# Kernel optimization log

Hardware: AMD Instinct MI355X
Metric: run time of the kernel (lower is better)

## Reference

```python
import jax, jax.numpy as jnp
import numpy as np

N_KEYS, PER_KEY = 8, 6
NUM_CONCEPTS = N_KEYS * PER_KEY  # 48
NUM_CLASS = 7
D_VIT, D = 768, 512
LOGIT_SCALE = 100.0


def adaptive_avg_pool_matrix(L_in: int, L_out: int) -> np.ndarray:
    """Linear operator replicating torch AdaptiveAvgPool1d: out[i] = mean(x[start_i:end_i])."""
    M = np.zeros((L_in, L_out), dtype=np.float32)
    for i in range(L_out):
        s = (i * L_in) // L_out
        e = -(((-(i + 1)) * L_in) // L_out)  # ceil((i+1)*L_in/L_out)
        M[s:e, i] = 1.0 / (e - s)
    return M


def setup_inputs() -> dict:
    key = jax.random.key(0)
    ks = jax.random.split(key, 12)
    feats = jax.random.normal(ks[0], (12, 32, 197, D_VIT), dtype=jnp.float32)
    # frozen text-side concept embeddings (CLIP text feats are ~unit norm, 512-d)
    ce = jax.random.normal(ks[1], (NUM_CONCEPTS, D), dtype=jnp.float32)
    concept_embeds = ce / jnp.linalg.norm(ce, axis=-1, keepdims=True)
    sc = 1.0 / np.sqrt(D_VIT)
    W_lin = jax.random.normal(ks[2], (D, D_VIT), dtype=jnp.float32) * sc
    b_lin = jnp.zeros((D,), dtype=jnp.float32)
    W_proj = jax.random.normal(ks[3], (D, D_VIT), dtype=jnp.float32) * sc
    scg = 1.0 / np.sqrt(3 * D)
    W_gate = jax.random.normal(ks[4], (D, 3 * D), dtype=jnp.float32) * scg
    b_gate = jnp.zeros((D,), dtype=jnp.float32)
    scu = 1.0 / np.sqrt(2 * D)
    W_upd = jax.random.normal(ks[5], (D, 2 * D), dtype=jnp.float32) * scu
    b_upd = jnp.zeros((D,), dtype=jnp.float32)
    W_cls = jax.random.normal(ks[6], (NUM_CLASS, NUM_CONCEPTS), dtype=jnp.float32) / np.sqrt(NUM_CONCEPTS)
    b_cls = jnp.zeros((NUM_CLASS,), dtype=jnp.float32)
    return {
        'feats': feats, 'concept_embeds': concept_embeds,
        'W_lin': W_lin, 'b_lin': b_lin, 'W_proj': W_proj,
        'W_gate': W_gate, 'b_gate': b_gate, 'W_upd': W_upd, 'b_upd': b_upd,
        'W_cls': W_cls, 'b_cls': b_cls,
    }


def _forward(feats, concept_embeds, W_lin, b_lin, W_proj, W_gate, b_gate, W_upd, b_upd, W_cls, b_cls):
    L, B, S, _ = feats.shape
    M = jnp.asarray(adaptive_avg_pool_matrix(S - 1, NUM_CONCEPTS))  # [196, 48]
    q0 = jnp.broadcast_to(concept_embeds[None], (B, NUM_CONCEPTS, D))

    def step(q, f):  # f: [B, 197, 768]
        cls_tok = f[:, :1, :]                                  # [B,1,768]
        pooled = jnp.einsum('bjd,ji->bid', f[:, 1:, :], M)     # [B,48,768]
        vt = jnp.concatenate([cls_tok, pooled], axis=1) @ W_lin.T + b_lin  # [B,49,512]
        attn = jax.nn.softmax(jnp.einsum('bqd,bvd->bqv', q, vt), axis=-1)
        fuse = jnp.einsum('bqv,bvd->bqd', attn, vt)            # [B,48,512]
        cls_ctx = jnp.broadcast_to(cls_tok @ W_proj.T, q.shape)
        gate = jax.nn.sigmoid(jnp.concatenate([fuse, q, cls_ctx], -1) @ W_gate.T + b_gate)
        upd = jnp.tanh(jnp.concatenate([fuse, q], -1) @ W_upd.T + b_upd)
        return gate * q + (1.0 - gate) * upd, fuse

    _, trace = jax.lax.scan(step, q0, feats)                   # trace: [12,B,48,512]

    last = trace[-1]
    vision_semantic = last / jnp.maximum(jnp.linalg.norm(last, axis=-1, keepdims=True), 1e-12)
    vs = vision_semantic.reshape(B, N_KEYS, PER_KEY, D)
    anchors = concept_embeds.reshape(N_KEYS, PER_KEY, D)
    image_logits = (LOGIT_SCALE * jnp.einsum('bkpd,kqd->bkpq', vs, anchors).mean(axis=2)).reshape(B, NUM_CONCEPTS)
    cls_logits = image_logits @ W_cls.T + b_cls
    diffs = trace[1:] - jax.lax.stop_gradient(trace[:-1])
    loss_consistency = jnp.sum(jnp.mean(diffs * diffs, axis=(1, 2, 3)))
    return cls_logits, image_logits, loss_consistency


def reference(feats, concept_embeds, W_lin, b_lin, W_proj, W_gate, b_gate, W_upd, b_upd, W_cls, b_cls):
    return _forward(feats, concept_embeds, W_lin, b_lin, W_proj, W_gate, b_gate, W_upd, b_upd, W_cls, b_cls)
```

## Files before the change

kernel.cpp:

```cpp
#include <hip/hip_runtime.h>
#include <hip/hip_bf16.h>

#define LL 12
#define BB 32
#define SS 197
#define DV 768
#define DD 512
#define CC 48
#define VV 49
#define LOSS_DEN 786432.0f

typedef unsigned short u16;
typedef unsigned int u32;
using bf16x8 = __attribute__((ext_vector_type(8))) __bf16;
using f32x4 = __attribute__((ext_vector_type(4))) float;
using u16x8 = __attribute__((ext_vector_type(8))) u16;
using u16x4 = __attribute__((ext_vector_type(4))) u16;

__device__ __forceinline__ u16 bf16h(float x) {
    u32 u = __builtin_bit_cast(u32, x);
    return (u16)((u + 0x7FFFu + ((u >> 16) & 1u)) >> 16);
}
__device__ __forceinline__ float bf2f(u16 h) {
    u32 u = ((u32)h) << 16;
    return __builtin_bit_cast(float, u);
}
__device__ __forceinline__ f32x4 mfma16(bf16x8 a, bf16x8 b, f32x4 c) {
    return __builtin_amdgcn_mfma_f32_16x16x32_bf16(a, b, c, 0, 0, 0);
}
__device__ __forceinline__ void gl_lds16(const void* g, void* s) {
    __builtin_amdgcn_global_load_lds((const __attribute__((address_space(1))) u32*)g,
                                     (__attribute__((address_space(3))) u32*)s, 16, 0, 0);
}

#define NLW (512 * 768)
#define NGW (512 * 1536)
#define NUW (512 * 1024)
#define CTX_BLKS 48
#define POOL2_BLKS (LL * BB * 2)
#define WSPLIT4_BLKS ((NLW + NGW + NUW) / 1024)
#define INITQ8_BLKS ((BB * CC * DD) / 2048)

__device__ __forceinline__ void gemm_f32_tile(const float* __restrict__ A, int lda,
                                              const float* __restrict__ W, int wstride, int K,
                                              const float* __restrict__ bias,
                                              float* __restrict__ Cout,
                                              int m0, int n0, int t, float* AsB, float* BsB) {
    float (*As)[65] = (float(*)[65])AsB;
    float (*Bs)[65] = (float(*)[65])BsB;
    int r = t >> 2;
    int kc = (t & 3) * 8;
    int tx = t & 15, ty = t >> 4;
    float acc[4][4] = {};
    for (int k0 = 0; k0 < K; k0 += 32) {
        const float4* pa = (const float4*)(A + (size_t)(m0 + r) * lda + k0 + kc);
        float4 a0 = pa[0], a1 = pa[1];
        const float4* pw = (const float4*)(W + (size_t)(n0 + r) * wstride + k0 + kc);
        float4 w0 = pw[0], w1 = pw[1];
        As[kc + 0][r] = a0.x; As[kc + 1][r] = a0.y; As[kc + 2][r] = a0.z; As[kc + 3][r] = a0.w;
        As[kc + 4][r] = a1.x; As[kc + 5][r] = a1.y; As[kc + 6][r] = a1.z; As[kc + 7][r] = a1.w;
        Bs[kc + 0][r] = w0.x; Bs[kc + 1][r] = w0.y; Bs[kc + 2][r] = w0.z; Bs[kc + 3][r] = w0.w;
        Bs[kc + 4][r] = w1.x; Bs[kc + 5][r] = w1.y; Bs[kc + 6][r] = w1.z; Bs[kc + 7][r] = w1.w;
        __syncthreads();
#pragma unroll
        for (int kk = 0; kk < 32; ++kk) {
            float a[4], b[4];
#pragma unroll
            for (int i = 0; i < 4; ++i) { a[i] = As[kk][ty * 4 + i]; b[i] = Bs[kk][tx * 4 + i]; }
#pragma unroll
            for (int i = 0; i < 4; ++i)
#pragma unroll
                for (int j = 0; j < 4; ++j) acc[i][j] += a[i] * b[j];
        }
        __syncthreads();
    }
#pragma unroll
    for (int i = 0; i < 4; ++i) {
        int m = m0 + ty * 4 + i;
#pragma unroll
        for (int j = 0; j < 4; ++j) {
            int n = n0 + tx * 4 + j;
            Cout[(size_t)m * DD + n] = acc[i][j] + (bias ? bias[n] : 0.0f);
        }
    }
}

__global__ __launch_bounds__(256) void mega_pre(const float* __restrict__ feats,
                                                const float* __restrict__ Wl,
                                                const float* __restrict__ Wg,
                                                const float* __restrict__ Wu,
                                                const float* __restrict__ Wp,
                                                const float* __restrict__ ce,
                                                u16* __restrict__ Xh, u16* __restrict__ Xl,
                                                u16* Wlh, u16* Wll, u16* Wgh, u16* Wgl,
                                                u16* Wuh, u16* Wul,
                                                u16* __restrict__ qh, u16* __restrict__ ql,
                                                float* __restrict__ loss,
                                                float* __restrict__ ctx) {
    __shared__ float smf[2 * 32 * 65];
    int bid = blockIdx.x;
    int t = threadIdx.x;
    if (bid < CTX_BLKS) {
        gemm_f32_tile(feats, SS * DV, Wp, DV, DV, nullptr, ctx,
                      (bid >> 3) * 64, (bid & 7) * 64, t, smf, smf + 32 * 65);
    } else if (bid < CTX_BLKS + POOL2_BLKS) {
        if (t >= 192) return;
        int pb = bid - CTX_BLKS;
        int lb = pb >> 1, half = pb & 1;
        const float4* fb = (const float4*)(feats + (size_t)lb * SS * DV);
        size_t xbase = (size_t)lb * VV * DV + 4 * t;
        if (half == 0) {
            float4 c = fb[t];
            float cv[4] = {c.x, c.y, c.z, c.w};
            u16x4 hh, ll2;
#pragma unroll
            for (int j = 0; j < 4; ++j) {
                u16 h = bf16h(cv[j]);
                hh[j] = h;
                ll2[j] = bf16h(cv[j] - bf2f(h));
            }
            *(u16x4*)(Xh + xbase) = hh;
            *(u16x4*)(Xl + xbase) = ll2;
        }
        int ib0 = half * 24, ib1 = ib0 + 24;
        for (int i = ib0; i < ib1; ++i) {
            int s = (i * 196) / 48;
            int e = ((i + 1) * 196 + 47) / 48;
            float4 acc = {0.f, 0.f, 0.f, 0.f};
            for (int j = s; j < e; ++j) {
                float4 v = fb[(size_t)(1 + j) * 192 + t];
                acc.x += v.x; acc.y += v.y; acc.z += v.z; acc.w += v.w;
            }
            float inv = 1.0f / (float)(e - s);
            float av[4] = {acc.x * inv, acc.y * inv, acc.z * inv, acc.w * inv};
            u16x4 hh, ll2;
#pragma unroll
            for (int j = 0; j < 4; ++j) {
                u16 h = bf16h(av[j]);
                hh[j] = h;
                ll2[j] = bf16h(av[j] - bf2f(h));
            }
            size_t o = xbase + (size_t)(1 + i) * DV;
            *(u16x4*)(Xh + o) = hh;
            *(u16x4*)(Xl + o) = ll2;
        }
    } else if (bid < CTX_BLKS + POOL2_BLKS + WSPLIT4_BLKS) {
        int i = ((bid - CTX_BLKS - POOL2_BLKS) * 256 + t) * 4;
        float4 v;
        u16 *ph, *pl;
        int j;
        if (i < NLW) { v = *(const float4*)(Wl + i); ph = Wlh; pl = Wll; j = i; }
        else if (i < NLW + NGW) { j = i - NLW; v = *(const float4*)(Wg + j); ph = Wgh; pl = Wgl; }
        else { j = i - NLW - NGW; v = *(const float4*)(Wu + j); ph = Wuh; pl = Wul; }
        float vv[4] = {v.x, v.y, v.z, v.w};
        u16x4 hh, ll2;
#pragma unroll
        for (int k = 0; k < 4; ++k) {
            u16 h = bf16h(vv[k]);
            hh[k] = h;
            ll2[k] = bf16h(vv[k] - bf2f(h));
        }
        *(u16x4*)(ph + j) = hh;
        *(u16x4*)(pl + j) = ll2;
    } else {
        int i8 = ((bid - CTX_BLKS - POOL2_BLKS - WSPLIT4_BLKS) * 256 + t) * 8;
        int src = i8 % (CC * DD);
        float4 a = *(const float4*)(ce + src);
        float4 b2 = *(const float4*)(ce + src + 4);
        float vv[8] = {a.x, a.y, a.z, a.w, b2.x, b2.y, b2.z, b2.w};
        u16x8 hh, ll2;
#pragma unroll
        for (int k = 0; k < 8; ++k) {
            u16 h = bf16h(vv[k]);
            hh[k] = h;
            ll2[k] = bf16h(vv[k] - bf2f(h));
        }
        *(u16x8*)(qh + i8) = hh;
        *(u16x8*)(ql + i8) = ll2;
        if (i8 == 0) loss[0] = 0.0f;
    }
}

__global__ __launch_bounds__(256, 2) void vt_gemm(const u16* __restrict__ Xh, const u16* __restrict__ Xl,
                                                  const u16* __restrict__ Wh, const u16* __restrict__ Wl,
                                                  const float* __restrict__ bias,
                                                  float* __restrict__ vtf,
                                                  const float* __restrict__ ctx,
                                                  const float* __restrict__ Wg,
                                                  const float* __restrict__ bg,
                                                  float* __restrict__ Cg) {
    __shared__ u16 sm[24576];
    int tid = threadIdx.x;
    if (blockIdx.x >= 1176) {
        int b2 = blockIdx.x - 1176;
        gemm_f32_tile(ctx, DD, Wg + 1024, 1536, DD, bg, Cg,
                      (b2 >> 3) * 64, (b2 & 7) * 64, tid, (float*)sm, (float*)sm + 32 * 65);
        return;
    }
    int w = tid >> 6, l = tid & 63, lr = l & 15, ls = l >> 4;
    int i = blockIdx.x, m, n;
    if (i < 1152) { int a = i >> 6, r2 = i & 63; m = 8 * a + (r2 & 7); n = r2 >> 3; }
    else { int j = i - 1152; m = 144 + (j >> 3); n = j & 7; }
    int m0 = m * 128, n0 = n * 64;
    f32x4 acc[2][4];
#pragma unroll
    for (int ii = 0; ii < 2; ++ii)
#pragma unroll
        for (int j = 0; j < 4; ++j) acc[ii][j] = f32x4{0.f, 0.f, 0.f, 0.f};

    auto stage = [&](u16* dst, int k0) {
#pragma unroll
        for (int is = 0; is < 6; ++is) {
            int q = is * 256 + tid;
            const u16* src;
            int off;
            if (is < 2)      { int qr = q;        int row = qr >> 2, sl = qr & 3; src = Xh + (size_t)(m0 + row) * DV + k0 + ((sl ^ ((row >> 1) & 3)) << 3); off = qr * 8; }
            else if (is < 4) { int qr = q - 512;  int row = qr >> 2, sl = qr & 3; src = Xl + (size_t)(m0 + row) * DV + k0 + ((sl ^ ((row >> 1) & 3)) << 3); off = 4096 + qr * 8; }
            else if (is < 5) { int qr = q - 1024; int row = qr >> 2, sl = qr & 3; src = Wh + (size_t)(n0 + row) * DV + k0 + ((sl ^ ((row >> 1) & 3)) << 3); off = 8192 + qr * 8; }
            else             { int qr = q - 1280; int row = qr >> 2, sl = qr & 3; src = Wl + (size_t)(n0 + row) * DV + k0 + ((sl ^ ((row >> 1) & 3)) << 3); off = 10240 + qr * 8; }
            gl_lds16(src, dst + off);
        }
    };

    stage(sm, 0);
    __syncthreads();
    for (int t = 0; t < 24; ++t) {
        u16* cur = sm + ((t & 1) ? 12288 : 0);
        u16* nxt = sm + ((t & 1) ? 0 : 12288);
        if (t + 1 < 24) stage(nxt, (t + 1) * 32);
        bf16x8 ah[2], al2[2], bh[4], bl2[4];
#pragma unroll
        for (int rf = 0; rf < 2; ++rf) {
            int row = 32 * w + 16 * rf + lr;
            int ro = row * 32 + ((ls ^ ((row >> 1) & 3)) << 3);
            ah[rf] = *(const bf16x8*)(cur + ro);
            al2[rf] = *(const bf16x8*)(cur + 4096 + ro);
        }
#pragma unroll
        for (int cf = 0; cf < 4; ++cf) {
            int nn = 16 * cf + lr;
            int no = nn * 32 + ((ls ^ ((nn >> 1) & 3)) << 3);
            bh[cf] = *(const bf16x8*)(cur + 8192 + no);
            bl2[cf] = *(const bf16x8*)(cur + 10240 + no);
        }
#pragma unroll
        for (int rf = 0; rf < 2; ++rf)
#pragma unroll
            for (int cf = 0; cf < 4; ++cf) {
                acc[rf][cf] = mfma16(ah[rf], bh[cf], acc[rf][cf]);
                acc[rf][cf] = mfma16(ah[rf], bl2[cf], acc[rf][cf]);
                acc[rf][cf] = mfma16(al2[rf], bh[cf], acc[rf][cf]);
            }
        __syncthreads();
    }
#pragma unroll
    for (int rf = 0; rf < 2; ++rf)
#pragma unroll
        for (int cf = 0; cf < 4; ++cf)
#pragma unroll
            for (int r = 0; r < 4; ++r) {
                int row = m0 + 32 * w + 16 * rf + 4 * ls + r;
                int col = n0 + 16 * cf + lr;
                vtf[(size_t)row * DD + col] = acc[rf][cf][r] + bias[col];
            }
}

__device__ __forceinline__ void gemm32x64(u16* sm, const u16* Ah,
                                          const u16* Wgh, const u16* Wuh,
                                          int m0, int n0, int tid,
                                          f32x4 accg[2], f32x4 accu[2]) {
    int w = tid >> 6, lane = tid & 63, lr = lane & 15, ls = lane >> 4;
    auto stage = [&](u16* buf, int k0) {
        {
            int j = tid, row = j >> 3, sl = j & 7;
            int ko = k0 + ((sl ^ (row & 7)) << 3);
            gl_lds16(Ah + (size_t)(m0 + row) * DD + ko, buf + j * 8);
        }
#pragma unroll
        for (int i2 = 0; i2 < 4; ++i2) {
            int aidx = tid + 256 * i2;
            int arr = aidx >> 9, j = aidx & 511;
            int row = j >> 3, sl = j & 7;
            int ko = k0 + ((sl ^ (row & 7)) << 3);
            const u16* src = arr ? (Wuh + (size_t)(n0 + row) * 1024 + ko)
                                 : (Wgh + (size_t)(n0 + row) * 1536 + ko);
            gl_lds16(src, buf + 2048 + arr * 4096 + j * 8);
        }
    };
    stage(sm, 0);
    __syncthreads();
    for (int t = 0; t < 8; ++t) {
        u16* cur = sm + (t & 1) * 10240;
        if (t + 1 < 8) stage(sm + ((t + 1) & 1) * 10240, (t + 1) * 64);
#pragma unroll
        for (int ks = 0; ks < 2; ++ks) {
            int slot = ks * 4 + ls;
            int n = 16 * w + lr;
            int bo = n * 64 + ((slot ^ (n & 7)) << 3);
            bf16x8 gh8 = *(const bf16x8*)(cur + 2048 + bo);
            bf16x8 uh8 = *(const bf16x8*)(cur + 6144 + bo);
#pragma unroll
            for (int rf = 0; rf < 2; ++rf) {
                int r = 16 * rf + lr;
                int ao = r * 64 + ((slot ^ (r & 7)) << 3);
                bf16x8 ah8 = *(const bf16x8*)(cur + ao);
                accg[rf] = mfma16(ah8, gh8, accg[rf]);
                accu[rf] = mfma16(ah8, uh8, accu[rf]);
            }
        }
        __syncthreads();
    }
}

__global__ __launch_bounds__(256, 3) void attn_qpart(
    const u16* __restrict__ qh, const u16* __restrict__ ql,
    const float* __restrict__ vtL,
    float* __restrict__ fcur, const float* __restrict__ fprev,
    u16* __restrict__ fh, u16* __restrict__ fl,
    float* __restrict__ loss, int do_loss,
    const u16* __restrict__ Wgh, const u16* __restrict__ Wuh,
    float* __restrict__ qg, float* __restrict__ qu) {
    __shared__ u16 sm[20480];
    int tid = threadIdx.x;
    if (blockIdx.x < 192) {
        int wgid = blockIdx.x * 4 + (tid >> 6);
        int lane = tid & 63;
        int b = wgid / 24;
        int r0 = b * CC + (wgid % 24) * 2;
        size_t o0 = (size_t)r0 * DD + lane * 8;
        u16x8 h0 = *(const u16x8*)(qh + o0), g0 = *(const u16x8*)(ql + o0);
        u16x8 h1 = *(const u16x8*)(qh + o0 + DD), g1 = *(const u16x8*)(ql + o0 + DD);
        float q0v[8], q1v[8];
#pragma unroll
        for (int j = 0; j < 8; ++j) {
            q0v[j] = bf2f(h0[j]) + bf2f(g0[j]);
            q1v[j] = bf2f(h1[j]) + bf2f(g1[j]);
        }
        const float* vf = vtL + (size_t)b * VV * DD + lane * 8;
        float m0 = -3e38f, m1 = -3e38f, s0 = 0.f, s1 = 0.f;
        float a0[8] = {}, a1[8] = {};
        for (int v = 0; v < VV; ++v) {
            float4 r0v = *(const float4*)(vf + (size_t)v * DD);
            float4 r1v = *(const float4*)(vf + (size_t)v * DD + 4);
            float rv[8] = {r0v.x, r0v.y, r0v.z, r0v.w, r1v.x, r1v.y, r1v.z, r1v.w};
            float p0 = 0.f, p1 = 0.f;
#pragma unroll
            for (int j = 0; j < 8; ++j) { p0 += q0v[j] * rv[j]; p1 += q1v[j] * rv[j]; }
#pragma unroll
            for (int off = 32; off > 0; off >>= 1) { p0 += __shfl_xor(p0, off); p1 += __shfl_xor(p1, off); }
            float nm0 = fmaxf(m0, p0);
            float sc0 = __expf(m0 - nm0), w0 = __expf(p0 - nm0);
            s0 = s0 * sc0 + w0;
            float nm1 = fmaxf(m1, p1);
            float sc1 = __expf(m1 - nm1), w1 = __expf(p1 - nm1);
            s1 = s1 * sc1 + w1;
#pragma unroll
            for (int j = 0; j < 8; ++j) {
                a0[j] = a0[j] * sc0 + w0 * rv[j];
                a1[j] = a1[j] * sc1 + w1 * rv[j];
            }
            m0 = nm0;
            m1 = nm1;
        }
        float inv0 = 1.0f / s0, inv1 = 1.0f / s1;
        float d2 = 0.f;
        float f0v[8], f1v[8];
        u16x8 oh0, ol0, oh1, ol1;
#pragma unroll
        for (int j = 0; j < 8; ++j) {
            float f = a0[j] * inv0;
            f0v[j] = f;
            u16 hh = bf16h(f);
            oh0[j] = hh;
            ol0[j] = bf16h(f - bf2f(hh));
            float f2 = a1[j] * inv1;
            f1v[j] = f2;
            u16 h2 = bf16h(f2);
            oh1[j] = h2;
            ol1[j] = bf16h(f2 - bf2f(h2));
        }
        *(float4*)(fcur + o0) = float4{f0v[0], f0v[1], f0v[2], f0v[3]};
        *(float4*)(fcur + o0 + 4) = float4{f0v[4], f0v[5], f0v[6], f0v[7]};
        *(float4*)(fcur + o0 + DD) = float4{f1v[0], f1v[1], f1v[2], f1v[3]};
        *(float4*)(fcur + o0 + DD + 4) = float4{f1v[4], f1v[5], f1v[6], f1v[7]};
        *(u16x8*)(fh + o0) = oh0;
        *(u16x8*)(fl + o0) = ol0;
        *(u16x8*)(fh + o0 + DD) = oh1;
        *(u16x8*)(fl + o0 + DD) = ol1;
        if (do_loss) {
#pragma unroll
            for (int j = 0; j < 8; ++j) {
                float d = f0v[j] - fprev[o0 + j];
                d2 += d * d;
                float e = f1v[j] - fprev[o0 + DD + j];
                d2 += e * e;
            }
#pragma unroll
            for (int off = 32; off > 0; off >>= 1) d2 += __shfl_xor(d2, off);
            if (lane == 0) atomicAdd(loss, d2);
        }
    } else {
        int tb = blockIdx.x - 192;
        int m0 = (tb >> 3) * 32, n0 = (tb & 7) * 64;
        f32x4 accg[2], accu[2];
#pragma unroll
        for (int i = 0; i < 2; ++i) { accg[i] = f32x4{0.f, 0.f, 0.f, 0.f}; accu[i] = f32x4{0.f, 0.f, 0.f, 0.f}; }
        gemm32x64(sm, qh, Wgh + 512, Wuh + 512, m0, n0, tid, accg, accu);
        int w = tid >> 6, lane = tid & 63, lr = lane & 15, ls = lane >> 4;
#pragma unroll
        for (int rf = 0; rf < 2; ++rf)
#pragma unroll
            for (int r = 0; r < 4; ++r) {
                int row = m0 + 16 * rf + 4 * ls + r;
                int col = n0 + 16 * w + lr;
                size_t o = (size_t)row * DD + col;
                qg[o] = accg[rf][r];
                qu[o] = accu[rf][r];
            }
    }
}

__global__ __launch_bounds__(256, 3) void fusepart(
    const u16* __restrict__ fhp,
    const u16* __restrict__ qhp, const u16* __restrict__ qlp,
    const u16* __restrict__ Wgh, const u16* __restrict__ Wuh,
    const float* __restrict__ qg, const float* __restrict__ qu,
    const float* __restrict__ CgL, const float* __restrict__ bu,
    u16* __restrict__ qoh, u16* __restrict__ qol) {
    __shared__ u16 sm[20480];
    int tid = threadIdx.x;
    int m0 = (blockIdx.x >> 3) * 32, n0 = (blockIdx.x & 7) * 64;
    f32x4 accg[2], accu[2];
#pragma unroll
    for (int i = 0; i < 2; ++i) { accg[i] = f32x4{0.f, 0.f, 0.f, 0.f}; accu[i] = f32x4{0.f, 0.f, 0.f, 0.f}; }
    gemm32x64(sm, fhp, Wgh, Wuh, m0, n0, tid, accg, accu);
    int w = tid >> 6, lane = tid & 63, lr = lane & 15, ls = lane >> 4;
#pragma unroll
    for (int rf = 0; rf < 2; ++rf)
#pragma unroll
        for (int r = 0; r < 4; ++r) {
            int row = m0 + 16 * rf + 4 * ls + r;
            int col = n0 + 16 * w + lr;
            int b = row / CC;
            size_t o = (size_t)row * DD + col;
            float gpre = accg[rf][r] + qg[o] + CgL[(size_t)b * DD + col];
            float upre = accu[rf][r] + qu[o] + bu[col];
            float g = 1.0f / (1.0f + __expf(-gpre));
            float u = tanhf(upre);
            float qv = bf2f(qhp[o]) + bf2f(qlp[o]);
            float qo = g * qv + (1.0f - g) * u;
            u16 hh = bf16h(qo);
            qoh[o] = hh;
            qol[o] = bf16h(qo - bf2f(hh));
        }
}

__global__ __launch_bounds__(256) void final_kernel(const float* __restrict__ fuse_last,
                                                    const float* __restrict__ ce,
                                                    const float* __restrict__ W_cls,
                                                    const float* __restrict__ b_cls,
                                                    const float* __restrict__ loss_acc,
                                                    float* __restrict__ out) {
    int b = blockIdx.x;
    int t = threadIdx.x;
    int w = t >> 6, lane = t & 63;
    __shared__ float invn[CC];
    __shared__ float img[CC];
    const float* fb = fuse_last + (size_t)b * CC * DD;
    for (int c = w; c < CC; c += 4) {
        const float* fr = fb + (size_t)c * DD + lane * 8;
        float4 a0 = *(const float4*)fr;
        float4 a1 = *(const float4*)(fr + 4);
        float ss = a0.x * a0.x + a0.y * a0.y + a0.z * a0.z + a0.w * a0.w +
                   a1.x * a1.x + a1.y * a1.y + a1.z * a1.z + a1.w * a1.w;
#pragma unroll
        for (int off = 32; off > 0; off >>= 1) ss += __shfl_xor(ss, off);
        if (lane == 0) invn[c] = 1.0f / fmaxf(sqrtf(ss), 1e-12f);
    }
    __syncthreads();
    for (int g = w; g < CC; g += 4) {
        int k = g / 6;
        const float* ar = ce + (size_t)g * DD + lane * 8;
        float4 c0 = *(const float4*)ar;
        float4 c1 = *(const float4*)(ar + 4);
        float av[8] = {c0.x, c0.y, c0.z, c0.w, c1.x, c1.y, c1.z, c1.w};
        float accp = 0.0f;
        for (int p = 0; p < 6; ++p) {
            int row = k * 6 + p;
            const float* fr = fb + (size_t)row * DD + lane * 8;
            float4 f0 = *(const float4*)fr;
            float4 f1 = *(const float4*)(fr + 4);
            float fv[8] = {f0.x, f0.y, f0.z, f0.w, f1.x, f1.y, f1.z, f1.w};
            float d = 0.0f;
#pragma unroll
            for (int j = 0; j < 8; ++j) d += fv[j] * av[j];
            accp += d * invn[row];
        }
#pragma unroll
        for (int off = 32; off > 0; off >>= 1) accp += __shfl_xor(accp, off);
        if (lane == 0) img[g] = accp * (100.0f / 6.0f);
    }
    __syncthreads();
    if (t < CC) out[BB * 7 + b * CC + t] = img[t];
    if (t < 7) {
        float sacc = b_cls[t];
        for (int c = 0; c < CC; ++c) sacc += img[c] * W_cls[t * CC + c];
        out[b * 7 + t] = sacc;
    }
    if (b == 0 && t == 0) out[BB * 7 + BB * CC] = loss_acc[0] * (1.0f / LOSS_DEN);
}

extern "C" void kernel_launch(void* const* d_in, const int* in_sizes, int n_in,
                              void* d_out, int out_size, void* d_ws, size_t ws_size,
                              hipStream_t stream) {
    const float* feats = (const float*)d_in[0];
    const float* ce = (const float*)d_in[1];
    const float* W_lin = (const float*)d_in[2];
    const float* b_lin = (const float*)d_in[3];
    const float* W_proj = (const float*)d_in[4];
    const float* W_gate = (const float*)d_in[5];
    const float* b_gate = (const float*)d_in[6];
    const float* W_upd = (const float*)d_in[7];
    const float* b_upd = (const float*)d_in[8];
    const float* W_cls = (const float*)d_in[9];
    const float* b_cls = (const float*)d_in[10];
    float* out = (float*)d_out;

    char* base = (char*)d_ws;
    size_t off = 0;
    auto alloc = [&](size_t bytes) -> char* {
        char* r = base + off;
        off += (bytes + 255) & ~(size_t)255;
        return r;
    };
    u16* Xh = (u16*)alloc((size_t)LL * BB * VV * DV * 2);
    u16* Xl = (u16*)alloc((size_t)LL * BB * VV * DV * 2);
    float* vtf = (float*)alloc((size_t)LL * BB * VV * DD * 4);
    float* ctx = (float*)alloc((size_t)LL * BB * DD * 4);
    float* Cg = (float*)alloc((size_t)LL * BB * DD * 4);
    float* fbuf0 = (float*)alloc((size_t)BB * CC * DD * 4);
    float* fbuf1 = (float*)alloc((size_t)BB * CC * DD * 4);
    float* qg = (float*)alloc((size_t)BB * CC * DD * 4);
    float* qu = (float*)alloc((size_t)BB * CC * DD * 4);
    float* loss = (float*)alloc(256);
    u16* Wlh = (u16*)alloc((size_t)NLW * 2);
    u16* Wll = (u16*)alloc((size_t)NLW * 2);
    u16* Wgh = (u16*)alloc((size_t)NGW * 2);
    u16* Wgl = (u16*)alloc((size_t)NGW * 2);
    u16* Wuh = (u16*)alloc((size_t)NUW * 2);
    u16* Wul = (u16*)alloc((size_t)NUW * 2);
    u16* fh = (u16*)alloc((size_t)BB * CC * DD * 2);
    u16* fl = (u16*)alloc((size_t)BB * CC * DD * 2);
    u16* qah = (u16*)alloc((size_t)BB * CC * DD * 2);
    u16* qal = (u16*)alloc((size_t)BB * CC * DD * 2);
    u16* qbh = (u16*)alloc((size_t)BB * CC * DD * 2);
    u16* qbl = (u16*)alloc((size_t)BB * CC * DD * 2);
    u16* qph[2] = {qah, qbh};
    u16* qpl[2] = {qal, qbl};

    mega_pre<<<CTX_BLKS + POOL2_BLKS + WSPLIT4_BLKS + INITQ8_BLKS, 256, 0, stream>>>(
        feats, W_lin, W_gate, W_upd, W_proj, ce, Xh, Xl, Wlh, Wll, Wgh, Wgl, Wuh, Wul,
        qah, qal, loss, ctx);
    vt_gemm<<<1176 + CTX_BLKS, 256, 0, stream>>>(Xh, Xl, Wlh, Wll, b_lin, vtf,
                                                 ctx, W_gate, b_gate, Cg);

    int qc = 0;
    for (int l = 0; l < LL; ++l) {
        float* fcur = (l & 1) ? fbuf1 : fbuf0;
        const float* fprev = (l & 1) ? fbuf0 : fbuf1;
        int grid = (l < LL - 1) ? 576 : 192;
        attn_qpart<<<grid, 256, 0, stream>>>(qph[qc], qpl[qc],
                                             vtf + (size_t)l * BB * VV * DD,
                                             fcur, fprev, fh, fl, loss, l > 0 ? 1 : 0,
                                             Wgh, Wuh, qg, qu);
        if (l < LL - 1) {
            fusepart<<<384, 256, 0, stream>>>(fh, qph[qc], qpl[qc],
                                              Wgh, Wuh, qg, qu,
                                              Cg + (size_t)l * BB * DD, b_upd,
                                              qph[qc ^ 1], qpl[qc ^ 1]);
            qc ^= 1;
        }
    }

    final_kernel<<<BB, 256, 0, stream>>>((LL - 1) & 1 ? fbuf1 : fbuf0, ce, W_cls, b_cls, loss, out);
}
```

Before: 798.4 us.

## Precompose gate/update weights with W_lin to hoist fuse projections out of recurrence

Since fuse is linear in the vision tokens, the gate and update contributions of fuse are rewritten as attention over pre-projected tokens VG/VU. These come from combined weights W_gate·W_lin and W_upd·W_lin, computed once in a larger batched GEMM. The per-layer fusepart kernel is removed, and each layer becomes a single layer_step kernel that rebuilds q from the previous step's pre-activations. This trades per-layer serial GEMMs for a bigger up-front parallel GEMM and more memory traffic, and the combined weights use single bf16 precision, which risks accuracy.

```diff
diff --git a/kernel.cpp b/kernel.cpp
--- a/kernel.cpp
+++ b/kernel.cpp
@@ -37,6 +37,8 @@
 #define NGW (512 * 1536)
 #define NUW (512 * 1024)
 #define CTX_BLKS 48
+#define WCOMB_BLKS 96
+#define BIAS_BLKS 1
 #define POOL2_BLKS (LL * BB * 2)
 #define WSPLIT4_BLKS ((NLW + NGW + NUW) / 1024)
 #define INITQ8_BLKS ((BB * CC * DD) / 2048)
@@ -85,27 +87,94 @@
     }
 }
 
+__device__ __forceinline__ void gemm_f32_nn(const float* __restrict__ A, int lda,
+                                            const float* __restrict__ B, int ldb, int K,
+                                            u16* __restrict__ Cbf, int ldc,
+                                            int m0, int n0, int t, float* AsB, float* BsB) {
+    float (*As)[65] = (float(*)[65])AsB;
+    float (*Bs)[68] = (float(*)[68])BsB;
+    int tx = t & 15, ty = t >> 4;
+    float acc[4][4] = {};
+    for (int k0 = 0; k0 < K; k0 += 32) {
+        {
+            int r = t >> 2, kc = (t & 3) * 8;
+            const float4* pa = (const float4*)(A + (size_t)(m0 + r) * lda + k0 + kc);
+            float4 a0 = pa[0], a1 = pa[1];
+            As[kc + 0][r] = a0.x; As[kc + 1][r] = a0.y; As[kc + 2][r] = a0.z; As[kc + 3][r] = a0.w;
+            As[kc + 4][r] = a1.x; As[kc + 5][r] = a1.y; As[kc + 6][r] = a1.z; As[kc + 7][r] = a1.w;
+        }
+        {
+            int kr = t >> 3, jc = (t & 7) * 8;
+            const float4* pb = (const float4*)(B + (size_t)(k0 + kr) * ldb + n0 + jc);
+            float4 b0 = pb[0], b1 = pb[1];
+            Bs[kr][jc + 0] = b0.x; Bs[kr][jc + 1] = b0.y; Bs[kr][jc + 2] = b0.z; Bs[kr][jc + 3] = b0.w;
+            Bs[kr][jc + 4] = b1.x; Bs[kr][jc + 5] = b1.y; Bs[kr][jc + 6] = b1.z; Bs[kr][jc + 7] = b1.w;
+        }
+        __syncthreads();
+#pragma unroll
+        for (int kk = 0; kk < 32; ++kk) {
+            float a[4], b[4];
+#pragma unroll
+            for (int i = 0; i < 4; ++i) { a[i] = As[kk][ty * 4 + i]; b[i] = Bs[kk][tx * 4 + i]; }
+#pragma unroll
+            for (int i = 0; i < 4; ++i)
+#pragma unroll
+                for (int j = 0; j < 4; ++j) acc[i][j] += a[i] * b[j];
+        }
+        __syncthreads();
+    }
+#pragma unroll
+    for (int i = 0; i < 4; ++i)
+#pragma unroll
+        for (int j = 0; j < 4; ++j)
+            Cbf[(size_t)(m0 + ty * 4 + i) * ldc + n0 + tx * 4 + j] = bf16h(acc[i][j]);
+}
+
 __global__ __launch_bounds__(256) void mega_pre(const float* __restrict__ feats,
                                                 const float* __restrict__ Wl,
                                                 const float* __restrict__ Wg,
                                                 const float* __restrict__ Wu,
                                                 const float* __restrict__ Wp,
+                                                const float* __restrict__ bl,
+                                                const float* __restrict__ bg,
+                                                const float* __restrict__ buv,
                                                 const float* __restrict__ ce,
                                                 u16* __restrict__ Xh, u16* __restrict__ Xl,
-                                                u16* Wlh, u16* Wll, u16* Wgh, u16* Wgl,
-                                                u16* Wuh, u16* Wul,
+                                                u16* Wlh, u16* Wll, u16* Wgh, u16* Wuh,
+                                                u16* Wcg, u16* Wcu,
+                                                float* __restrict__ bg2, float* __restrict__ bu2,
                                                 u16* __restrict__ qh, u16* __restrict__ ql,
                                                 float* __restrict__ loss,
                                                 float* __restrict__ ctx) {
-    __shared__ float smf[2 * 32 * 65];
+    __shared__ float smf[32 * 65 + 32 * 68];
     int bid = blockIdx.x;
     int t = threadIdx.x;
     if (bid < CTX_BLKS) {
         gemm_f32_tile(feats, SS * DV, Wp, DV, DV, nullptr, ctx,
                       (bid >> 3) * 64, (bid & 7) * 64, t, smf, smf + 32 * 65);
-    } else if (bid < CTX_BLKS + POOL2_BLKS) {
+    } else if (bid < CTX_BLKS + 2 * WCOMB_BLKS) {
+        int b2 = bid - CTX_BLKS;
+        int which = b2 >= WCOMB_BLKS;
+        int b3 = b2 - which * WCOMB_BLKS;
+        int m0 = (b3 / 12) * 64, n0 = (b3 % 12) * 64;
+        if (which == 0)
+            gemm_f32_nn(Wg, 1536, Wl, DV, 512, Wcg, DV, m0, n0, t, smf, smf + 32 * 65);
+        else
+            gemm_f32_nn(Wu, 1024, Wl, DV, 512, Wcu, DV, m0, n0, t, smf, smf + 32 * 65);
+    } else if (bid < CTX_BLKS + 2 * WCOMB_BLKS + BIAS_BLKS) {
+        for (int n = t; n < 512; n += 256) {
+            float sg = bg[n], su = buv[n];
+            for (int k = 0; k < 512; ++k) {
+                float blv = bl[k];
+                sg += Wg[(size_t)n * 1536 + k] * blv;
+                su += Wu[(size_t)n * 1024 + k] * blv;
+            }
+            bg2[n] = sg;
+            bu2[n] = su;
+        }
+    } else if (bid < CTX_BLKS + 2 * WCOMB_BLKS + BIAS_BLKS + POOL2_BLKS) {
         if (t >= 192) return;
-        int pb = bid - CTX_BLKS;
+        int pb = bid - CTX_BLKS - 2 * WCOMB_BLKS - BIAS_BLKS;
         int lb = pb >> 1, half = pb & 1;
         const float4* fb = (const float4*)(feats + (size_t)lb * SS * DV);
         size_t xbase = (size_t)lb * VV * DV + 4 * t;
@@ -144,14 +213,14 @@
             *(u16x4*)(Xh + o) = hh;
             *(u16x4*)(Xl + o) = ll2;
         }
-    } else if (bid < CTX_BLKS + POOL2_BLKS + WSPLIT4_BLKS) {
-        int i = ((bid - CTX_BLKS - POOL2_BLKS) * 256 + t) * 4;
+    } else if (bid < CTX_BLKS + 2 * WCOMB_BLKS + BIAS_BLKS + POOL2_BLKS + WSPLIT4_BLKS) {
+        int i = ((bid - CTX_BLKS - 2 * WCOMB_BLKS - BIAS_BLKS - POOL2_BLKS) * 256 + t) * 4;
         float4 v;
-        u16 *ph, *pl;
+        u16 *ph, *pl = nullptr;
         int j;
         if (i < NLW) { v = *(const float4*)(Wl + i); ph = Wlh; pl = Wll; j = i; }
-        else if (i < NLW + NGW) { j = i - NLW; v = *(const float4*)(Wg + j); ph = Wgh; pl = Wgl; }
-        else { j = i - NLW - NGW; v = *(const float4*)(Wu + j); ph = Wuh; pl = Wul; }
+        else if (i < NLW + NGW) { j = i - NLW; v = *(const float4*)(Wg + j); ph = Wgh; }
+        else { j = i - NLW - NGW; v = *(const float4*)(Wu + j); ph = Wuh; }
         float vv[4] = {v.x, v.y, v.z, v.w};
         u16x4 hh, ll2;
 #pragma unroll
@@ -161,9 +230,9 @@
             ll2[k] = bf16h(vv[k] - bf2f(h));
         }
         *(u16x4*)(ph + j) = hh;
-        *(u16x4*)(pl + j) = ll2;
+        if (pl) *(u16x4*)(pl + j) = ll2;
     } else {
-        int i8 = ((bid - CTX_BLKS - POOL2_BLKS - WSPLIT4_BLKS) * 256 + t) * 8;
+        int i8 = ((bid - CTX_BLKS - 2 * WCOMB_BLKS - BIAS_BLKS - POOL2_BLKS - WSPLIT4_BLKS) * 256 + t) * 8;
         int src = i8 % (CC * DD);
         float4 a = *(const float4*)(ce + src);
         float4 b2 = *(const float4*)(ce + src + 4);
@@ -181,24 +250,28 @@
     }
 }
 
-__global__ __launch_bounds__(256, 2) void vt_gemm(const u16* __restrict__ Xh, const u16* __restrict__ Xl,
-                                                  const u16* __restrict__ Wh, const u16* __restrict__ Wl,
-                                                  const float* __restrict__ bias,
-                                                  float* __restrict__ vtf,
-                                                  const float* __restrict__ ctx,
-                                                  const float* __restrict__ Wg,
-                                                  const float* __restrict__ bg,
-                                                  float* __restrict__ Cg) {
+__global__ __launch_bounds__(256, 2) void big_gemm(const u16* __restrict__ Xh, const u16* __restrict__ Xl,
+                                                   const u16* __restrict__ Wh, const u16* __restrict__ Wl,
+                                                   const float* __restrict__ bias,
+                                                   float* __restrict__ vtf,
+                                                   const u16* __restrict__ Wcg, const u16* __restrict__ Wcu,
+                                                   float* __restrict__ VG, float* __restrict__ VU,
+                                                   const float* __restrict__ ctx,
+                                                   const float* __restrict__ Wg,
+                                                   const float* __restrict__ bg2,
+                                                   float* __restrict__ Cg) {
     __shared__ u16 sm[24576];
     int tid = threadIdx.x;
-    if (blockIdx.x >= 1176) {
-        int b2 = blockIdx.x - 1176;
-        gemm_f32_tile(ctx, DD, Wg + 1024, 1536, DD, bg, Cg,
+    if (blockIdx.x >= 3528) {
+        int b2 = blockIdx.x - 3528;
+        gemm_f32_tile(ctx, DD, Wg + 1024, 1536, DD, bg2, Cg,
                       (b2 >> 3) * 64, (b2 & 7) * 64, tid, (float*)sm, (float*)sm + 32 * 65);
         return;
     }
+    int sub = blockIdx.x / 1176;
+    int i = blockIdx.x % 1176;
     int w = tid >> 6, l = tid & 63, lr = l & 15, ls = l >> 4;
-    int i = blockIdx.x, m, n;
+    int m, n;
     if (i < 1152) { int a = i >> 6, r2 = i & 63; m = 8 * a + (r2 & 7); n = r2 >> 3; }
     else { int j = i - 1152; m = 144 + (j >> 3); n = j & 7; }
     int m0 = m * 128, n0 = n * 64;
@@ -208,137 +281,181 @@
 #pragma unroll
         for (int j = 0; j < 4; ++j) acc[ii][j] = f32x4{0.f, 0.f, 0.f, 0.f};
 
-    auto stage = [&](u16* dst, int k0) {
-#pragma unroll
-        for (int is = 0; is < 6; ++is) {
-            int q = is * 256 + tid;
-            const u16* src;
-            int off;
-            if (is < 2)      { int qr = q;        int row = qr >> 2, sl = qr & 3; src = Xh + (size_t)(m0 + row) * DV + k0 + ((sl ^ ((row >> 1) & 3)) << 3); off = qr * 8; }
-            else if (is < 4) { int qr = q - 512;  int row = qr >> 2, sl = qr & 3; src = Xl + (size_t)(m0 + row) * DV + k0 + ((sl ^ ((row >> 1) & 3)) << 3); off = 4096 + qr * 8; }
-            else if (is < 5) { int qr = q - 1024; int row = qr >> 2, sl = qr & 3; src = Wh + (size_t)(n0 + row) * DV + k0 + ((sl ^ ((row >> 1) & 3)) << 3); off = 8192 + qr * 8; }
-            else             { int qr = q - 1280; int row = qr >> 2, sl = qr & 3; src = Wl + (size_t)(n0 + row) * DV + k0 + ((sl ^ ((row >> 1) & 3)) << 3); off = 10240 + qr * 8; }
-            gl_lds16(src, dst + off);
+    if (sub == 0) {
+        auto stage = [&](u16* dst, int k0) {
+#pragma unroll
+            for (int is = 0; is < 6; ++is) {
+                int q = is * 256 + tid;
+                const u16* src;
+                int off;
+                if (is < 2)      { int qr = q;        int row = qr >> 2, sl = qr & 3; src = Xh + (size_t)(m0 + row) * DV + k0 + ((sl ^ ((row >> 1) & 3)) << 3); off = qr * 8; }
+                else if (is < 4) { int qr = q - 512;  int row = qr >> 2, sl = qr & 3; src = Xl + (size_t)(m0 + row) * DV + k0 + ((sl ^ ((row >> 1) & 3)) << 3); off = 4096 + qr * 8; }
+                else if (is < 5) { int qr = q - 1024; int row = qr >> 2, sl = qr & 3; src = Wh + (size_t)(n0 + row) * DV + k0 + ((sl ^ ((row >> 1) & 3)) << 3); off = 8192 + qr * 8; }
+                else             { int qr = q - 1280; int row = qr >> 2, sl = qr & 3; src = Wl + (size_t)(n0 + row) * DV + k0 + ((sl ^ ((row >> 1) & 3)) << 3); off = 10240 + qr * 8; }
+                gl_lds16(src, dst + off);
+            }
+        };
+        stage(sm, 0);
+        __syncthreads();
+        for (int t = 0; t < 24; ++t) {
+            u16* cur = sm + ((t & 1) ? 12288 : 0);
+            if (t + 1 < 24) stage(sm + ((t & 1) ? 0 : 12288), (t + 1) * 32);
+            bf16x8 ah[2], al2[2], bh[4], bl2[4];
+#pragma unroll
+            for (int rf = 0; rf < 2; ++rf) {
+                int row = 32 * w + 16 * rf + lr;
+                int ro = row * 32 + ((ls ^ ((row >> 1) & 3)) << 3);
+                ah[rf] = *(const bf16x8*)(cur + ro);
+                al2[rf] = *(const bf16x8*)(cur + 4096 + ro);
+            }
+#pragma unroll
+            for (int cf = 0; cf < 4; ++cf) {
+                int nn = 16 * cf + lr;
+                int no = nn * 32 + ((ls ^ ((nn >> 1) & 3)) << 3);
+                bh[cf] = *(const bf16x8*)(cur + 8192 + no);
+                bl2[cf] = *(const bf16x8*)(cur + 10240 + no);
+            }
+#pragma unroll
+            for (int rf = 0; rf < 2; ++rf)
+#pragma unroll
+                for (int cf = 0; cf < 4; ++cf) {
+                    acc[rf][cf] = mfma16(ah[rf], bh[cf], acc[rf][cf]);
+                    acc[rf][cf] = mfma16(ah[rf], bl2[cf], acc[rf][cf]);
+                    acc[rf][cf] = mfma16(al2[rf], bh[cf], acc[rf][cf]);
+                }
+            __syncthreads();
+        }
+#pragma unroll
+        for (int rf = 0; rf < 2; ++rf)
+#pragma unroll
+            for (int cf = 0; cf < 4; ++cf)
+#pragma unroll
+                for (int r = 0; r < 4; ++r) {
+                    int row = m0 + 32 * w + 16 * rf + 4 * ls + r;
+                    int col = n0 + 16 * cf + lr;
+                    vtf[(size_t)row * DD + col] = acc[rf][cf][r] + bias[col];
+                }
+    } else {
+        const u16* Wc = (sub == 1) ? Wcg : Wcu;
+        float* Out = (sub == 1) ? VG : VU;
+        auto stage = [&](u16* dst, int k0) {
+#pragma unroll
+            for (int is = 0; is < 2; ++is) {
+                int q = is * 256 + tid;
+                int row = q >> 2, sl = q & 3;
+                gl_lds16(Xh + (size_t)(m0 + row) * DV + k0 + ((sl ^ ((row >> 1) & 3)) << 3), dst + q * 8);
+            }
+            {
+                int row = tid >> 2, sl = tid & 3;
+                gl_lds16(Wc + (size_t)(n0 + row) * DV + k0 + ((sl ^ ((row >> 1) & 3)) << 3), dst + 4096 + tid * 8);
+            }
+        };
+        stage(sm, 0);
+        __syncthreads();
+        for (int t = 0; t < 24; ++t) {
+            u16* cur = sm + (t & 1) * 6144;
+            if (t + 1 < 24) stage(sm + ((t + 1) & 1) * 6144, (t + 1) * 32);
+            bf16x8 ah[2], bh[4];
+#pragma unroll
+            for (int rf = 0; rf < 2; ++rf) {
+                int row = 32 * w + 16 * rf + lr;
+                ah[rf] = *(const bf16x8*)(cur + row * 32 + ((ls ^ ((row >> 1) & 3)) << 3));
+            }
+#pragma unroll
+            for (int cf = 0; cf < 4; ++cf) {
+                int nn = 16 * cf + lr;
+                bh[cf] = *(const bf16x8*)(cur + 4096 + nn * 32 + ((ls ^ ((nn >> 1) & 3)) << 3));
+            }
+#pragma unroll
+            for (int rf = 0; rf < 2; ++rf)
+#pragma unroll
+                for (int cf = 0; cf < 4; ++cf)
+                    acc[rf][cf] = mfma16(ah[rf], bh[cf], acc[rf][cf]);
+            __syncthreads();
+        }
+#pragma unroll
+        for (int rf = 0; rf < 2; ++rf)
+#pragma unroll
+            for (int cf = 0; cf < 4; ++cf)
+#pragma unroll
+                for (int r = 0; r < 4; ++r) {
+                    int row = m0 + 32 * w + 16 * rf + 4 * ls + r;
+                    int col = n0 + 16 * cf + lr;
+                    Out[(size_t)row * DD + col] = acc[rf][cf][r];
+                }
+    }
+}
+
+__global__ __launch_bounds__(256, 2) void layer_step(
+    const u16* __restrict__ qph, const u16* __restrict__ qpl,
+    const float* __restrict__ gpgP, const float* __restrict__ gpuP,
+    const float* __restrict__ qgP, const float* __restrict__ quP,
+    const float* __restrict__ vtL, const float* __restrict__ vgL, const float* __restrict__ vuL,
+    const float* __restrict__ CgL, const float* __restrict__ bu2,
+    float* __restrict__ fcur, const float* __restrict__ fprev, float* __restrict__ loss,
+    int do_loss, int first, int last,
+    u16* __restrict__ qoh, u16* __restrict__ qol,
+    float* __restrict__ gpgO, float* __restrict__ gpuO,
+    const u16* __restrict__ Wgh, const u16* __restrict__ Wuh,
+    float* __restrict__ qgO, float* __restrict__ quO) {
+    __shared__ u16 sm[32768];
+    int tid = threadIdx.x;
+
+    auto recon8 = [&](size_t o, float out[8]) {
+        u16x8 ph = *(const u16x8*)(qph + o), pl = *(const u16x8*)(qpl + o);
+        if (first) {
+#pragma unroll
+            for (int j = 0; j < 8; ++j) out[j] = bf2f(ph[j]) + bf2f(pl[j]);
+        } else {
+            float4 g0 = *(const float4*)(gpgP + o), g1 = *(const float4*)(gpgP + o + 4);
+            float4 u0 = *(const float4*)(gpuP + o), u1 = *(const float4*)(gpuP + o + 4);
+            float4 a0 = *(const float4*)(qgP + o), a1 = *(const float4*)(qgP + o + 4);
+            float4 b0 = *(const float4*)(quP + o), b1 = *(const float4*)(quP + o + 4);
+            float gg[8] = {g0.x, g0.y, g0.z, g0.w, g1.x, g1.y, g1.z, g1.w};
+            float uu[8] = {u0.x, u0.y, u0.z, u0.w, u1.x, u1.y, u1.z, u1.w};
+            float ag[8] = {a0.x, a0.y, a0.z, a0.w, a1.x, a1.y, a1.z, a1.w};
+            float bb[8] = {b0.x, b0.y, b0.z, b0.w, b1.x, b1.y, b1.z, b1.w};
+#pragma unroll
+            for (int j = 0; j < 8; ++j) {
+                float g = 1.0f / (1.0f + __expf(-(gg[j] + ag[j])));
+                float u = tanhf(uu[j] + bb[j]);
+                float qp = bf2f(ph[j]) + bf2f(pl[j]);
+                out[j] = g * qp + (1.0f - g) * u;
+            }
         }
     };
 
-    stage(sm, 0);
-    __syncthreads();
-    for (int t = 0; t < 24; ++t) {
-        u16* cur = sm + ((t & 1) ? 12288 : 0);
-        u16* nxt = sm + ((t & 1) ? 0 : 12288);
-        if (t + 1 < 24) stage(nxt, (t + 1) * 32);
-        bf16x8 ah[2], al2[2], bh[4], bl2[4];
-#pragma unroll
-        for (int rf = 0; rf < 2; ++rf) {
-            int row = 32 * w + 16 * rf + lr;
-            int ro = row * 32 + ((ls ^ ((row >> 1) & 3)) << 3);
-            ah[rf] = *(const bf16x8*)(cur + ro);
-            al2[rf] = *(const bf16x8*)(cur + 4096 + ro);
-        }
-#pragma unroll
-        for (int cf = 0; cf < 4; ++cf) {
-            int nn = 16 * cf + lr;
-            int no = nn * 32 + ((ls ^ ((nn >> 1) & 3)) << 3);
-            bh[cf] = *(const bf16x8*)(cur + 8192 + no);
-            bl2[cf] = *(const bf16x8*)(cur + 10240 + no);
-        }
-#pragma unroll
-        for (int rf = 0; rf < 2; ++rf)
-#pragma unroll
-            for (int cf = 0; cf < 4; ++cf) {
-                acc[rf][cf] = mfma16(ah[rf], bh[cf], acc[rf][cf]);
-                acc[rf][cf] = mfma16(ah[rf], bl2[cf], acc[rf][cf]);
-                acc[rf][cf] = mfma16(al2[rf], bh[cf], acc[rf][cf]);
-            }
-        __syncthreads();
-    }
-#pragma unroll
-    for (int rf = 0; rf < 2; ++rf)
-#pragma unroll
-        for (int cf = 0; cf < 4; ++cf)
-#pragma unroll
-            for (int r = 0; r < 4; ++r) {
-                int row = m0 + 32 * w + 16 * rf + 4 * ls + r;
-                int col = n0 + 16 * cf + lr;
-                vtf[(size_t)row * DD + col] = acc[rf][cf][r] + bias[col];
-            }
-}
-
-__device__ __forceinline__ void gemm32x64(u16* sm, const u16* Ah,
-                                          const u16* Wgh, const u16* Wuh,
-                                          int m0, int n0, int tid,
-                                          f32x4 accg[2], f32x4 accu[2]) {
-    int w = tid >> 6, lane = tid & 63, lr = lane & 15, ls = lane >> 4;
-    auto stage = [&](u16* buf, int k0) {
-        {
-            int j = tid, row = j >> 3, sl = j & 7;
-            int ko = k0 + ((sl ^ (row & 7)) << 3);
-            gl_lds16(Ah + (size_t)(m0 + row) * DD + ko, buf + j * 8);
-        }
-#pragma unroll
-        for (int i2 = 0; i2 < 4; ++i2) {
-            int aidx = tid + 256 * i2;
-            int arr = aidx >> 9, j = aidx & 511;
-            int row = j >> 3, sl = j & 7;
-            int ko = k0 + ((sl ^ (row & 7)) << 3);
-            const u16* src = arr ? (Wuh + (size_t)(n0 + row) * 1024 + ko)
-                                 : (Wgh + (size_t)(n0 + row) * 1536 + ko);
-            gl_lds16(src, buf + 2048 + arr * 4096 + j * 8);
-        }
-    };
-    stage(sm, 0);
-    __syncthreads();
-    for (int t = 0; t < 8; ++t) {
-        u16* cur = sm + (t & 1) * 10240;
-        if (t + 1 < 8) stage(sm + ((t + 1) & 1) * 10240, (t + 1) * 64);
-#pragma unroll
-        for (int ks = 0; ks < 2; ++ks) {
-            int slot = ks * 4 + ls;
-            int n = 16 * w + lr;
-            int bo = n * 64 + ((slot ^ (n & 7)) << 3);
-            bf16x8 gh8 = *(const bf16x8*)(cur + 2048 + bo);
-            bf16x8 uh8 = *(const bf16x8*)(cur + 6144 + bo);
-#pragma unroll
-            for (int rf = 0; rf < 2; ++rf) {
-                int r = 16 * rf + lr;
-                int ao = r * 64 + ((slot ^ (r & 7)) << 3);
-                bf16x8 ah8 = *(const bf16x8*)(cur + ao);
-                accg[rf] = mfma16(ah8, gh8, accg[rf]);
-                accu[rf] = mfma16(ah8, uh8, accu[rf]);
-            }
-        }
-        __syncthreads();
-    }
-}
-
-__global__ __launch_bounds__(256, 3) void attn_qpart(
-    const u16* __restrict__ qh, const u16* __restrict__ ql,
-    const float* __restrict__ vtL,
-    float* __restrict__ fcur, const float* __restrict__ fprev,
-    u16* __restrict__ fh, u16* __restrict__ fl,
-    float* __restrict__ loss, int do_loss,
-    const u16* __restrict__ Wgh, const u16* __restrict__ Wuh,
-    float* __restrict__ qg, float* __restrict__ qu) {
-    __shared__ u16 sm[20480];
-    int tid = threadIdx.x;
     if (blockIdx.x < 192) {
-        int wgid = blockIdx.x * 4 + (tid >> 6);
-        int lane = tid & 63;
-        int b = wgid / 24;
-        int r0 = b * CC + (wgid % 24) * 2;
+        int d = blockIdx.x;
+        int xcd = d & 7, tt = d >> 3;
+        int b = (tt / 6) * 8 + xcd, rg = tt % 6;
+        int wv = tid >> 6, lane = tid & 63;
+        int r0 = b * CC + rg * 8 + wv * 2;
         size_t o0 = (size_t)r0 * DD + lane * 8;
-        u16x8 h0 = *(const u16x8*)(qh + o0), g0 = *(const u16x8*)(ql + o0);
-        u16x8 h1 = *(const u16x8*)(qh + o0 + DD), g1 = *(const u16x8*)(ql + o0 + DD);
         float q0v[8], q1v[8];
-#pragma unroll
-        for (int j = 0; j < 8; ++j) {
-            q0v[j] = bf2f(h0[j]) + bf2f(g0[j]);
-            q1v[j] = bf2f(h1[j]) + bf2f(g1[j]);
+        recon8(o0, q0v);
+        recon8(o0 + DD, q1v);
+        if (!last) {
+            u16x8 h0, l0, h1, l1;
+#pragma unroll
+            for (int j = 0; j < 8; ++j) {
+                u16 h = bf16h(q0v[j]);
+                h0[j] = h;
+                l0[j] = bf16h(q0v[j] - bf2f(h));
+                u16 h2 = bf16h(q1v[j]);
+                h1[j] = h2;
+                l1[j] = bf16h(q1v[j] - bf2f(h2));
+            }
+            *(u16x8*)(qoh + o0) = h0;
+            *(u16x8*)(qol + o0) = l0;
+            *(u16x8*)(qoh + o0 + DD) = h1;
+            *(u16x8*)(qol + o0 + DD) = l1;
         }
         const float* vf = vtL + (size_t)b * VV * DD + lane * 8;
+        const float* gf = vgL + (size_t)b * VV * DD + lane * 8;
+        const float* uf = vuL + (size_t)b * VV * DD + lane * 8;
         float m0 = -3e38f, m1 = -3e38f, s0 = 0.f, s1 = 0.f;
-        float a0[8] = {}, a1[8] = {};
+        float af0[8] = {}, af1[8] = {}, ag0[8] = {}, ag1[8] = {}, au0[8] = {}, au1[8] = {};
         for (int v = 0; v < VV; ++v) {
             float4 r0v = *(const float4*)(vf + (size_t)v * DD);
             float4 r1v = *(const float4*)(vf + (size_t)v * DD + 4);
@@ -354,105 +471,145 @@
             float nm1 = fmaxf(m1, p1);
             float sc1 = __expf(m1 - nm1), w1 = __expf(p1 - nm1);
             s1 = s1 * sc1 + w1;
-#pragma unroll
-            for (int j = 0; j < 8; ++j) {
-                a0[j] = a0[j] * sc0 + w0 * rv[j];
-                a1[j] = a1[j] * sc1 + w1 * rv[j];
+            if (!last) {
+                float4 gv0 = *(const float4*)(gf + (size_t)v * DD);
+                float4 gv1 = *(const float4*)(gf + (size_t)v * DD + 4);
+                float4 uv0 = *(const float4*)(uf + (size_t)v * DD);
+                float4 uv1 = *(const float4*)(uf + (size_t)v * DD + 4);
+                float gv[8] = {gv0.x, gv0.y, gv0.z, gv0.w, gv1.x, gv1.y, gv1.z, gv1.w};
+                float uv[8] = {uv0.x, uv0.y, uv0.z, uv0.w, uv1.x, uv1.y, uv1.z, uv1.w};
+#pragma unroll
+                for (int j = 0; j < 8; ++j) {
+                    af0[j] = af0[j] * sc0 + w0 * rv[j];
+                    af1[j] = af1[j] * sc1 + w1 * rv[j];
+                    ag0[j] = ag0[j] * sc0 + w0 * gv[j];
+                    ag1[j] = ag1[j] * sc1 + w1 * gv[j];
+                    au0[j] = au0[j] * sc0 + w0 * uv[j];
+                    au1[j] = au1[j] * sc1 + w1 * uv[j];
+                }
+            } else {
+#pragma unroll
+                for (int j = 0; j < 8; ++j) {
+                    af0[j] = af0[j] * sc0 + w0 * rv[j];
+                    af1[j] = af1[j] * sc1 + w1 * rv[j];
+                }
             }
             m0 = nm0;
             m1 = nm1;
         }
         float inv0 = 1.0f / s0, inv1 = 1.0f / s1;
-        float d2 = 0.f;
         float f0v[8], f1v[8];
-        u16x8 oh0, ol0, oh1, ol1;
-#pragma unroll
-        for (int j = 0; j < 8; ++j) {
-            float f = a0[j] * inv0;
-            f0v[j] = f;
-            u16 hh = bf16h(f);
-            oh0[j] = hh;
-            ol0[j] = bf16h(f - bf2f(hh));
-            float f2 = a1[j] * inv1;
-            f1v[j] = f2;
-            u16 h2 = bf16h(f2);
-            oh1[j] = h2;
-            ol1[j] = bf16h(f2 - bf2f(h2));
-        }
+#pragma unroll
+        for (int j = 0; j < 8; ++j) { f0v[j] = af0[j] * inv0; f1v[j] = af1[j] * inv1; }
         *(float4*)(fcur + o0) = float4{f0v[0], f0v[1], f0v[2], f0v[3]};
         *(float4*)(fcur + o0 + 4) = float4{f0v[4], f0v[5], f0v[6], f0v[7]};
         *(float4*)(fcur + o0 + DD) = float4{f1v[0], f1v[1], f1v[2], f1v[3]};
         *(float4*)(fcur + o0 + DD + 4) = float4{f1v[4], f1v[5], f1v[6], f1v[7]};
-        *(u16x8*)(fh + o0) = oh0;
-        *(u16x8*)(fl + o0) = ol0;
-        *(u16x8*)(fh + o0 + DD) = oh1;
-        *(u16x8*)(fl + o0 + DD) = ol1;
         if (do_loss) {
+            float d2 = 0.f;
 #pragma unroll
             for (int j = 0; j < 8; ++j) {
-                float d = f0v[j] - fprev[o0 + j];
-                d2 += d * d;
-                float e = f1v[j] - fprev[o0 + DD + j];
-                d2 += e * e;
+                float dd = f0v[j] - fprev[o0 + j];
+                d2 += dd * dd;
+                float ee = f1v[j] - fprev[o0 + DD + j];
+                d2 += ee * ee;
             }
 #pragma unroll
             for (int off = 32; off > 0; off >>= 1) d2 += __shfl_xor(d2, off);
             if (lane == 0) atomicAdd(loss, d2);
+        }
+        if (!last) {
+            float4 c0 = *(const float4*)(CgL + (size_t)b * DD + lane * 8);
+            float4 c1 = *(const float4*)(CgL + (size_t)b * DD + lane * 8 + 4);
+            float cg[8] = {c0.x, c0.y, c0.z, c0.w, c1.x, c1.y, c1.z, c1.w};
+            float4 e0 = *(const float4*)(bu2 + lane * 8);
+            float4 e1 = *(const float4*)(bu2 + lane * 8 + 4);
+            float bv[8] = {e0.x, e0.y, e0.z, e0.w, e1.x, e1.y, e1.z, e1.w};
+            float og0[8], og1[8], ou0[8], ou1[8];
+#pragma unroll
+            for (int j = 0; j < 8; ++j) {
+                og0[j] = ag0[j] * inv0 + cg[j];
+                og1[j] = ag1[j] * inv1 + cg[j];
+                ou0[j] = au0[j] * inv0 + bv[j];
+                ou1[j] = au1[j] * inv1 + bv[j];
+            }
+            *(float4*)(gpgO + o0) = float4{og0[0], og0[1], og0[2], og0[3]};
+            *(float4*)(gpgO + o0 + 4) = float4{og0[4], og0[5], og0[6], og0[7]};
+            *(float4*)(gpgO + o0 + DD) = float4{og1[0], og1[1], og1[2], og1[3]};
+            *(float4*)(gpgO + o0 + DD + 4) = float4{og1[4], og1[5], og1[6], og1[7]};
+            *(float4*)(gpuO + o0) = float4{ou0[0], ou0[1], ou0[2], ou0[3]};
+            *(float4*)(gpuO + o0 + 4) = float4{ou0[4], ou0[5], ou0[6], ou0[7]};
+            *(float4*)(gpuO + o0 + DD) = float4{ou1[0], ou1[1], ou1[2], ou1[3]};
+            *(float4*)(gpuO + o0 + DD + 4) = float4{ou1[4], ou1[5], ou1[6], ou1[7]};
         }
     } else {
         int tb = blockIdx.x - 192;
         int m0 = (tb >> 3) * 32, n0 = (tb & 7) * 64;
+        for (int j = 0; j < 8; ++j) {
+            int e = j * 2048 + tid * 8;
+            int row = e >> 9, col = e & 511;
+            size_t o = (size_t)(m0 + row) * DD + col;
+            float qv[8];
+            recon8(o, qv);
+            u16x8 hv;
+#pragma unroll
+            for (int jj = 0; jj < 8; ++jj) hv[jj] = bf16h(qv[jj]);
+            int cslot = (col >> 3) & 7;
+            int addr = row * 512 + (col & ~63) + ((cslot ^ (row & 7)) << 3);
+            *(u16x8*)(sm + addr) = hv;
+        }
+        __syncthreads();
         f32x4 accg[2], accu[2];
 #pragma unroll
         for (int i = 0; i < 2; ++i) { accg[i] = f32x4{0.f, 0.f, 0.f, 0.f}; accu[i] = f32x4{0.f, 0.f, 0.f, 0.f}; }
-        gemm32x64(sm, qh, Wgh + 512, Wuh + 512, m0, n0, tid, accg, accu);
-        int w = tid >> 6, lane = tid & 63, lr = lane & 15, ls = lane >> 4;
+        int wv = tid >> 6, lane = tid & 63, lr = lane & 15, ls = lane >> 4;
+        u16* wbuf = sm + 16384;
+        auto stageW = [&](u16* buf, int k0) {
+#pragma unroll
+            for (int i2 = 0; i2 < 4; ++i2) {
+                int aidx = tid + 256 * i2;
+                int arr = aidx >> 9, jx = aidx & 511;
+                int row = jx >> 3, sl = jx & 7;
+                int ko = k0 + ((sl ^ (row & 7)) << 3);
+                const u16* src = arr ? (Wuh + (size_t)(n0 + row) * 1024 + 512 + ko)
+                                     : (Wgh + (size_t)(n0 + row) * 1536 + 512 + ko);
+                gl_lds16(src, buf + arr * 4096 + jx * 8);
+            }
+        };
+        stageW(wbuf, 0);
+        __syncthreads();
+        for (int t2 = 0; t2 < 8; ++t2) {
+            u16* cur = wbuf + (t2 & 1) * 8192;
+            if (t2 + 1 < 8) stageW(wbuf + ((t2 + 1) & 1) * 8192, (t2 + 1) * 64);
+#pragma unroll
+            for (int ks = 0; ks < 2; ++ks) {
+                int slot = ks * 4 + ls;
+                int n = 16 * wv + lr;
+                int bo = n * 64 + ((slot ^ (n & 7)) << 3);
+                bf16x8 gh8 = *(const bf16x8*)(cur + bo);
+                bf16x8 uh8 = *(const bf16x8*)(cur + 4096 + bo);
+#pragma unroll
+                for (int rf = 0; rf < 2; ++rf) {
+                    int r = 16 * rf + lr;
+                    int ao = r * 512 + t2 * 64 + ((slot ^ (r & 7)) << 3);
+                    bf16x8 ah8 = *(const bf16x8*)(sm + ao);
+                    accg[rf] = mfma16(ah8, gh8, accg[rf]);
+                    accu[rf] = mfma16(ah8, uh8, accu[rf]);
+                }
+            }
+            __syncthreads();
+        }
 #pragma unroll
         for (int rf = 0; rf < 2; ++rf)
 #pragma unroll
             for (int r = 0; r < 4; ++r) {
                 int row = m0 + 16 * rf + 4 * ls + r;
-                int col = n0 + 16 * w + lr;
+                int col = n0 + 16 * wv + lr;
                 size_t o = (size_t)row * DD + col;
-                qg[o] = accg[rf][r];
-                qu[o] = accu[rf][r];
-            }
-    }
-}
-
-__global__ __launch_bounds__(256, 3) void fusepart(
-    const u16* __restrict__ fhp,
-    const u16* __restrict__ qhp, const u16* __restrict__ qlp,
-    const u16* __restrict__ Wgh, const u16* __restrict__ Wuh,
-    const float* __restrict__ qg, const float* __restrict__ qu,
-    const float* __restrict__ CgL, const float* __restrict__ bu,
-    u16* __restrict__ qoh, u16* __restrict__ qol) {
-    __shared__ u16 sm[20480];
-    int tid = threadIdx.x;
-    int m0 = (blockIdx.x >> 3) * 32, n0 = (blockIdx.x & 7) * 64;
-    f32x4 accg[2], accu[2];
-#pragma unroll
-    for (int i = 0; i < 2; ++i) { accg[i] = f32x4{0.f, 0.f, 0.f, 0.f}; accu[i] = f32x4{0.f, 0.f, 0.f, 0.f}; }
-    gemm32x64(sm, fhp, Wgh, Wuh, m0, n0, tid, accg, accu);
-    int w = tid >> 6, lane = tid & 63, lr = lane & 15, ls = lane >> 4;
-#pragma unroll
-    for (int rf = 0; rf < 2; ++rf)
-#pragma unroll
-        for (int r = 0; r < 4; ++r) {
-            int row = m0 + 16 * rf + 4 * ls + r;
-            int col = n0 + 16 * w + lr;
-            int b = row / CC;
-            size_t o = (size_t)row * DD + col;
-            float gpre = accg[rf][r] + qg[o] + CgL[(size_t)b * DD + col];
-            float upre = accu[rf][r] + qu[o] + bu[col];
-            float g = 1.0f / (1.0f + __expf(-gpre));
-            float u = tanhf(upre);
-            float qv = bf2f(qhp[o]) + bf2f(qlp[o]);
-            float qo = g * qv + (1.0f - g) * u;
-            u16 hh = bf16h(qo);
-            qoh[o] = hh;
-            qol[o] = bf16h(qo - bf2f(hh));
-        }
+                qgO[o] = accg[rf][r];
+                quO[o] = accu[rf][r];
+            }
+    }
 }
 
 __global__ __launch_bounds__(256) void final_kernel(const float* __restrict__ fuse_last,
@@ -536,50 +693,56 @@
     u16* Xh = (u16*)alloc((size_t)LL * BB * VV * DV * 2);
     u16* Xl = (u16*)alloc((size_t)LL * BB * VV * DV * 2);
     float* vtf = (float*)alloc((size_t)LL * BB * VV * DD * 4);
+    float* VG = (float*)alloc((size_t)LL * BB * VV * DD * 4);
+    float* VU = (float*)alloc((size_t)LL * BB * VV * DD * 4);
     float* ctx = (float*)alloc((size_t)LL * BB * DD * 4);
     float* Cg = (float*)alloc((size_t)LL * BB * DD * 4);
     float* fbuf0 = (float*)alloc((size_t)BB * CC * DD * 4);
     float* fbuf1 = (float*)alloc((size_t)BB * CC * DD * 4);
-    float* qg = (float*)alloc((size_t)BB * CC * DD * 4);
-    float* qu = (float*)alloc((size_t)BB * CC * DD * 4);
+    float* gpg[2] = {(float*)alloc((size_t)BB * CC * DD * 4), (float*)alloc((size_t)BB * CC * DD * 4)};
+    float* gpu[2] = {(float*)alloc((size_t)BB * CC * DD * 4), (float*)alloc((size_t)BB * CC * DD * 4)};
+    float* qg[2] = {(float*)alloc((size_t)BB * CC * DD * 4), (float*)alloc((size_t)BB * CC * DD * 4)};
+    float* qu[2] = {(float*)alloc((size_t)BB * CC * DD * 4), (float*)alloc((size_t)BB * CC * DD * 4)};
     float* loss = (float*)alloc(256);
     u16* Wlh = (u16*)alloc((size_t)NLW * 2);
     u16* Wll = (u16*)alloc((size_t)NLW * 2);
     u16* Wgh = (u16*)alloc((size_t)NGW * 2);
-    u16* Wgl = (u16*)alloc((size_t)NGW * 2);
     u16* Wuh = (u16*)alloc((size_t)NUW * 2);
-    u16* Wul = (u16*)alloc((size_t)NUW * 2);
-    u16* fh = (u16*)alloc((size_t)BB * CC * DD * 2);
-    u16* fl = (u16*)alloc((size_t)BB * CC * DD * 2);
+    u16* Wcg = (u16*)alloc((size_t)512 * DV * 2);
+    u16* Wcu = (u16*)alloc((size_t)512 * DV * 2);
+    float* bg2 = (float*)alloc(512 * 4);
+    float* bu2 = (float*)alloc(512 * 4);
     u16* qah = (u16*)alloc((size_t)BB * CC * DD * 2);
     u16* qal = (u16*)alloc((size_t)BB * CC * DD * 2);
     u16* qbh = (u16*)alloc((size_t)BB * CC * DD * 2);
     u16* qbl = (u16*)alloc((size_t)BB * CC * DD * 2);
-    u16* qph[2] = {qah, qbh};
-    u16* qpl[2] = {qal, qbl};
-
-    mega_pre<<<CTX_BLKS + POOL2_BLKS + WSPLIT4_BLKS + INITQ8_BLKS, 256, 0, stream>>>(
-        feats, W_lin, W_gate, W_upd, W_proj, ce, Xh, Xl, Wlh, Wll, Wgh, Wgl, Wuh, Wul,
-        qah, qal, loss, ctx);
-    vt_gemm<<<1176 + CTX_BLKS, 256, 0, stream>>>(Xh, Xl, Wlh, Wll, b_lin, vtf,
-                                                 ctx, W_gate, b_gate, Cg);
-
-    int qc = 0;
+    u16* qPh[2] = {qah, qbh};
+    u16* qPl[2] = {qal, qbl};
+
+    int total_pre = CTX_BLKS + 2 * WCOMB_BLKS + BIAS_BLKS + POOL2_BLKS + WSPLIT4_BLKS + INITQ8_BLKS;
+    mega_pre<<<total_pre, 256, 0, stream>>>(feats, W_lin, W_gate, W_upd, W_proj,
+                                            b_lin, b_gate, b_upd, ce,
+                                            Xh, Xl, Wlh, Wll, Wgh, Wuh, Wcg, Wcu,
+                                            bg2, bu2, qah, qal, loss, ctx);
+    big_gemm<<<3576, 256, 0, stream>>>(Xh, Xl, Wlh, Wll, b_lin, vtf, Wcg, Wcu, VG, VU,
+                                       ctx, W_gate, bg2, Cg);
+
     for (int l = 0; l < LL; ++l) {
         float* fcur = (l & 1) ? fbuf1 : fbuf0;
         const float* fprev = (l & 1) ? fbuf0 : fbuf1;
-        int grid = (l < LL - 1) ? 576 : 192;
-        attn_qpart<<<grid, 256, 0, stream>>>(qph[qc], qpl[qc],
-                                             vtf + (size_t)l * BB * VV * DD,
-                                             fcur, fprev, fh, fl, loss, l > 0 ? 1 : 0,
-                                             Wgh, Wuh, qg, qu);
-        if (l < LL - 1) {
-            fusepart<<<384, 256, 0, stream>>>(fh, qph[qc], qpl[qc],
-                                              Wgh, Wuh, qg, qu,
-                                              Cg + (size_t)l * BB * DD, b_upd,
-                                              qph[qc ^ 1], qpl[qc ^ 1]);
-            qc ^= 1;
-        }
+        int last = (l == LL - 1) ? 1 : 0;
+        int first = (l == 0) ? 1 : 0;
+        int rd = (l + 1) & 1;
+        int wr2 = l & 1;
+        size_t loff = (size_t)l * BB * VV * DD;
+        layer_step<<<last ? 192 : 576, 256, 0, stream>>>(
+            qPh[l & 1], qPl[l & 1],
+            gpg[rd], gpu[rd], qg[rd], qu[rd],
+            vtf + loff, VG + loff, VU + loff,
+            Cg + (size_t)l * BB * DD, bu2,
+            fcur, fprev, loss, l > 0 ? 1 : 0, first, last,
+            qPh[(l + 1) & 1], qPl[(l + 1) & 1],
+            gpg[wr2], gpu[wr2], Wgh, Wuh, qg[wr2], qu[wr2]);
     }
 
     final_kernel<<<BB, 256, 0, stream>>>((LL - 1) & 1 ? fbuf1 : fbuf0, ce, W_cls, b_cls, loss, out);
```

Result: slower. 1.029 ms (+28.9%).
